# Kernel tuning notes

Measured on AMD Instinct MI355X. Metric: run time of the kernel, lower is better.

Reference implementation:

```python
import jax, jax.numpy as jnp
import numpy as np

N = 4096        # nodes
C = 256         # in_channels
E0 = 65536      # edges before adding self-loops
RATIO = 0.5
K = int(np.ceil(RATIO * N))   # pooled nodes (topk)
NEG = 0.2       # leaky relu negative slope


def setup_inputs() -> dict:
    key = jax.random.key(0)
    ks = jax.random.split(key, 12)
    x = jax.random.normal(ks[0], (N, C), jnp.float32)
    src = jax.random.randint(ks[1], (E0,), 0, N)
    off = jax.random.randint(ks[2], (E0,), 1, N)
    dst = (src + off) % N                      # guaranteed no self-loops
    edge_index = jnp.stack([src, dst]).astype(jnp.int32)
    s = 1.0 / np.sqrt(C)
    s2 = 1.0 / np.sqrt(2 * C)
    u = lambda k, shape, b: jax.random.uniform(k, shape, jnp.float32, -b, b)
    return dict(
        x=x, edge_index=edge_index,
        Wq=u(ks[3], (C, C), s), bq=u(ks[4], (C,), s),          # lin_q
        gat_w=u(ks[5], (2 * C,), s2), gat_b=u(ks[6], (1,), s2),  # gat_att
        le1_w=u(ks[7], (C,), s), le1_b=u(ks[8], (1,), s),      # LEConv lin1
        le2_w=u(ks[9], (C,), s),                                # LEConv lin2 (no bias)
        le3_w=u(ks[10], (C,), s), le3_b=u(ks[11], (1,), s),    # LEConv lin3
    )


def _asap(x, edge_index, Wq, bq, gat_w, gat_b, le1_w, le1_b, le2_w, le3_w, le3_b):
    # add_remaining_self_loops (inputs have none -> all N loops, weight 1)
    loops = jnp.arange(N, dtype=edge_index.dtype)
    ei = jnp.concatenate([edge_index, jnp.stack([loops, loops])], axis=1)
    i, j = ei[0], ei[1]          # i: aggregation target, j: neighbor

    x_pool = x                   # GNN is None -> x_pool = x
    xj = x_pool[j]               # [E, C]

    # Master2Token attention: X_q = scatter_max over target i
    Xq = jax.ops.segment_max(xj, i, num_segments=N)       # [N, C]
    Mq = Xq @ Wq + bq                                     # lin_q
    sc = jnp.concatenate([Mq[i], xj], axis=-1) @ gat_w + gat_b[0]  # [E]
    sc = jnp.where(sc > 0, sc, NEG * sc)                  # leaky relu

    # segment softmax over targets i
    m = jax.ops.segment_max(sc, i, num_segments=N)
    e = jnp.exp(sc - m[i])
    z = jax.ops.segment_sum(e, i, num_segments=N)
    score = e / z[i]                                      # dropout_att=0, eval

    # cluster representation
    out = jax.ops.segment_sum(x[j] * score[:, None], i, num_segments=N)  # [N, C]

    # fitness = sigmoid(LEConv(out)): x_i' = lin3(x_i) + sum_j (lin1(x_j) - lin2(x_i))
    a = out @ le1_w + le1_b[0]                            # [N]
    b = out @ le2_w                                       # [N]
    agg = jax.ops.segment_sum(a[j] - b[i], i, num_segments=N)
    fitness = jax.nn.sigmoid(agg + out @ le3_w + le3_b[0])  # [N]

    # topk pooling (single graph -> global top_k)
    fit_k, perm = jax.lax.top_k(fitness, K)
    x_out = out[perm] * fit_k[:, None]                    # [K, C]

    # graph_connectivity: E = S^T A S (dense stand-in for coalesce+spspmm)
    n_idx = jnp.zeros(N, jnp.int32).at[perm].set(jnp.arange(K, dtype=jnp.int32))
    in_perm = jnp.zeros(N, bool).at[perm].set(True)
    sS = jax.lax.stop_gradient(score) * in_perm[i]        # score.detach(), kept-cluster edges
    S = jnp.zeros((N, K), x.dtype).at[j, n_idx[i]].add(sS)   # S[j, new(i)] = score
    A = jnp.zeros((N, N), x.dtype).at[i, j].add(1.0)      # edge_weight None -> ones, coalesced
    Eadj = S.T @ (A @ S)                                  # [K, K]
    # remove_self_loops then add_remaining_self_loops(fill=1)
    Eadj = Eadj - jnp.diag(jnp.diag(Eadj)) + jnp.eye(K, dtype=Eadj.dtype)
    return x_out, Eadj, perm


def reference(x, edge_index, Wq, bq, gat_w, gat_b, le1_w, le1_b, le2_w, le3_w, le3_b):
    return _asap(x, edge_index, Wq, bq, gat_w, gat_b,
                 le1_w, le1_b, le2_w, le3_w, le3_b)
```

## Files before the change

### kernel.cpp

```cpp
#include <hip/hip_runtime.h>
#include <math.h>

constexpr int NN  = 4096;
constexpr int CC  = 256;
constexpr int EE0 = 65536;
constexpr int EE  = 69632;
constexpr int KK  = 2048;
constexpr int SL  = 128;

__device__ __forceinline__ void edge_ij(const int* __restrict__ ei, int e, int& i, int& j) {
    if (e < EE0) { i = ei[e]; j = ei[EE0 + e]; }
    else         { i = e - EE0; j = i; }
}

__global__ __launch_bounds__(256) void k_build(const int* __restrict__ ei,
                                               int* cnt_i, int* cnt_j,
                                               int* lsti_j, int* slot_ij, int* lstj_i,
                                               const float* __restrict__ x,
                                               const float* __restrict__ Wq, const float* __restrict__ bq,
                                               const float* __restrict__ gat_w, const float* __restrict__ gat_b,
                                               double* wv, double* consts, double* beta_node, int EB) {
    const int t = threadIdx.x, g = t >> 6, l = t & 63;
    if ((int)blockIdx.x < EB) {
        int e = blockIdx.x * 256 + t;
        if (e >= EE) return;
        int i, j; edge_ij(ei, e, i, j);
        int si = atomicAdd(&cnt_i[i], 1);
        int sj = atomicAdd(&cnt_j[j], 1);
        lsti_j[i * SL + si]  = j;
        slot_ij[i * SL + si] = j * SL + sj;
        lstj_i[j * SL + sj]  = i;
        return;
    }
    if ((int)blockIdx.x < EB + CC) {
        int k = blockIdx.x - EB;
        double s = (double)Wq[k * CC + t] * (double)gat_w[t];
        #pragma unroll
        for (int d = 32; d > 0; d >>= 1) s += __shfl_down(s, d, 64);
        __shared__ double red[4];
        if (l == 0) red[g] = s;
        __syncthreads();
        if (t == 0) wv[k] = red[0] + red[1] + red[2] + red[3];
        if (k == 0 && t == 0) {
            double cb = 0.0;
            for (int q = 0; q < CC; ++q) cb += (double)bq[q] * (double)gat_w[q];
            consts[0] = cb + (double)gat_b[0];
        }
        return;
    }
    int m = (blockIdx.x - EB - CC) * 4 + g;
    const float* gw2 = gat_w + CC;
    float4 v = ((const float4*)(x + (size_t)m * CC))[l];
    double s = (double)v.x * (double)gw2[4 * l]     + (double)v.y * (double)gw2[4 * l + 1]
             + (double)v.z * (double)gw2[4 * l + 2] + (double)v.w * (double)gw2[4 * l + 3];
    #pragma unroll
    for (int d = 32; d > 0; d >>= 1) s += __shfl_down(s, d, 64);
    if (l == 0) beta_node[m] = s;
}

__global__ __launch_bounds__(256) void k_attn(const float* __restrict__ x,
                                              const int* __restrict__ cnt_i, const int* __restrict__ lsti_j,
                                              const int* __restrict__ slot_ij,
                                              const int* __restrict__ cnt_j, const int* __restrict__ lstj_i,
                                              const double* __restrict__ wv, const double* __restrict__ beta_node,
                                              const double* __restrict__ consts,
                                              const float* __restrict__ le1_w, const float* __restrict__ le1_b,
                                              const float* __restrict__ le2_w,
                                              const float* __restrict__ le3_w, const float* __restrict__ le3_b,
                                              float* __restrict__ sval_i, float* __restrict__ svalj,
                                              float* __restrict__ out32,
                                              double* __restrict__ zlog) {
    __shared__ int    sj[SL];
    __shared__ double ssc[SL];
    __shared__ double mz[2];
    __shared__ double bcast;
    __shared__ union { float4 m4[4][64]; double d[4][CC]; } red;

    const int n = blockIdx.x, t = threadIdx.x, g = t >> 6, l = t & 63;
    const int base = n * SL;
    const int deg = cnt_i[n];

    for (int p = t; p < deg; p += 256) {
        int j = lsti_j[base + p];
        sj[p] = j;
        ssc[p] = beta_node[j];
    }
    __syncthreads();

    float4 mx = make_float4(-INFINITY, -INFINITY, -INFINITY, -INFINITY);
    for (int p = g; p < deg; p += 4) {
        float4 v = ((const float4*)(x + (size_t)sj[p] * CC))[l];
        mx.x = fmaxf(mx.x, v.x); mx.y = fmaxf(mx.y, v.y);
        mx.z = fmaxf(mx.z, v.z); mx.w = fmaxf(mx.w, v.w);
    }
    red.m4[g][l] = mx;
    __syncthreads();
    if (g == 0) {
        float4 a = red.m4[0][l], b = red.m4[1][l], c2 = red.m4[2][l], d4 = red.m4[3][l];
        float m0 = fmaxf(fmaxf(a.x, b.x), fmaxf(c2.x, d4.x));
        float m1 = fmaxf(fmaxf(a.y, b.y), fmaxf(c2.y, d4.y));
        float m2 = fmaxf(fmaxf(a.z, b.z), fmaxf(c2.z, d4.z));
        float m3 = fmaxf(fmaxf(a.w, b.w), fmaxf(c2.w, d4.w));
        double alph = (double)m0 * wv[4 * l]     + (double)m1 * wv[4 * l + 1]
                    + (double)m2 * wv[4 * l + 2] + (double)m3 * wv[4 * l + 3];
        #pragma unroll
        for (int dd = 32; dd > 0; dd >>= 1) alph += __shfl_down(alph, dd, 64);
        if (l == 0) mz[0] = alph + consts[0];
    }
    __syncthreads();
    double an = mz[0];
    for (int p = t; p < deg; p += 256) {
        double v = an + ssc[p];
        ssc[p] = v > 0.0 ? v : 0.2 * v;
    }
    __syncthreads();
    if (t < 64) {
        double mm = -1e300;
        for (int p = l; p < deg; p += 64) mm = fmax(mm, ssc[p]);
        #pragma unroll
        for (int d = 32; d > 0; d >>= 1) mm = fmax(mm, __shfl_xor(mm, d, 64));
        double z = 0.0;
        for (int p = l; p < deg; p += 64) z += exp(ssc[p] - mm);
        #pragma unroll
        for (int d = 32; d > 0; d >>= 1) z += __shfl_xor(z, d, 64);
        if (l == 0) { mz[0] = mm; mz[1] = 1.0 / z; }
    }
    __syncthreads();
    double mm = mz[0], inv = mz[1];
    for (int p = t; p < deg; p += 256) {
        double sc = exp(ssc[p] - mm) * inv;
        ssc[p] = sc;
        float scf = (float)sc;
        sval_i[base + p] = scf;
        svalj[slot_ij[base + p]] = scf;
    }
    __syncthreads();
    double a0 = 0, a1 = 0, a2 = 0, a3 = 0;
    for (int p = g; p < deg; p += 4) {
        double sc = ssc[p];
        float4 v = ((const float4*)(x + (size_t)sj[p] * CC))[l];
        a0 += sc * (double)v.x; a1 += sc * (double)v.y;
        a2 += sc * (double)v.z; a3 += sc * (double)v.w;
    }
    red.d[g][4 * l + 0] = a0; red.d[g][4 * l + 1] = a1;
    red.d[g][4 * l + 2] = a2; red.d[g][4 * l + 3] = a3;
    __syncthreads();
    if (g == 0) {
        double o0 = red.d[0][4*l]   + red.d[1][4*l]   + red.d[2][4*l]   + red.d[3][4*l];
        double o1 = red.d[0][4*l+1] + red.d[1][4*l+1] + red.d[2][4*l+1] + red.d[3][4*l+1];
        double o2 = red.d[0][4*l+2] + red.d[1][4*l+2] + red.d[2][4*l+2] + red.d[3][4*l+2];
        double o3 = red.d[0][4*l+3] + red.d[1][4*l+3] + red.d[2][4*l+3] + red.d[3][4*l+3];
        float4 ov; ov.x = (float)o0; ov.y = (float)o1; ov.z = (float)o2; ov.w = (float)o3;
        ((float4*)(out32 + (size_t)n * CC))[l] = ov;
        float4 w1 = ((const float4*)le1_w)[l];
        float4 w2 = ((const float4*)le2_w)[l];
        float4 w3 = ((const float4*)le3_w)[l];
        double s1 = o0 * (double)w1.x + o1 * (double)w1.y + o2 * (double)w1.z + o3 * (double)w1.w;
        double s2 = o0 * (double)w2.x + o1 * (double)w2.y + o2 * (double)w2.z + o3 * (double)w2.w;
        double s3 = o0 * (double)w3.x + o1 * (double)w3.y + o2 * (double)w3.z + o3 * (double)w3.w;
        #pragma unroll
        for (int dd = 32; dd > 0; dd >>= 1) {
            s1 += __shfl_down(s1, dd, 64);
            s2 += __shfl_down(s2, dd, 64);
            s3 += __shfl_down(s3, dd, 64);
        }
        if (l == 0) {
            double a64n = s1 + (double)le1_b[0];
            double b64n = s2;
            double l3vn = s3 + (double)le3_b[0];
            atomicAdd(&zlog[n], l3vn - (double)deg * b64n);
            bcast = a64n;
        }
    }
    __syncthreads();
    double a64n = bcast;
    int cj = cnt_j[n], jb = n * SL;
    for (int p = t; p < cj; p += 256) {
        atomicAdd(&zlog[lstj_i[jb + p]], a64n);
    }
}

__global__ __launch_bounds__(256) void k_rank(const double* __restrict__ zlog,
                                              const float* __restrict__ out32,
                                              int* __restrict__ perm, int* __restrict__ n_idx,
                                              float* __restrict__ xout, float* __restrict__ operm) {
    int n = blockIdx.x, t = threadIdx.x;
    double zn = zlog[n];
    int cnt = 0;
    #pragma unroll
    for (int u = 0; u < NN / 256; ++u) {
        int m = t + u * 256;
        double zm = zlog[m];
        cnt += ((zm > zn) || (zm == zn && m < n)) ? 1 : 0;
    }
    #pragma unroll
    for (int d = 32; d > 0; d >>= 1) cnt += __shfl_down(cnt, d, 64);
    __shared__ int red[4];
    __shared__ int rr;
    if ((t & 63) == 0) red[t >> 6] = cnt;
    __syncthreads();
    if (t == 0) {
        int r = red[0] + red[1] + red[2] + red[3];
        rr = r;
        if (r < KK) {
            perm[r] = n;
            n_idx[n] = r;
            operm[r] = (float)n;
        } else {
            n_idx[n] = -1;
        }
    }
    __syncthreads();
    int r = rr;
    if (r < KK) {
        double fit = 1.0 / (1.0 + exp(-zn));
        xout[(size_t)r * CC + t] = (float)((double)out32[(size_t)n * CC + t] * fit);
    }
}

__global__ __launch_bounds__(256) void k_eadj(const int* __restrict__ cnt_i, const int* __restrict__ lsti_j,
                                              const float* __restrict__ sval_i,
                                              const int* __restrict__ cnt_j, const int* __restrict__ lstj_i,
                                              const float* __restrict__ svalj,
                                              const int* __restrict__ n_idx,
                                              const int* __restrict__ perm,
                                              float* __restrict__ Ead) {
    __shared__ float row[KK];
    int r = blockIdx.x, t = threadIdx.x;
    float4 z4 = make_float4(0.f, 0.f, 0.f, 0.f);
    for (int c = t; c < KK / 4; c += 256) ((float4*)row)[c] = z4;
    __syncthreads();
    int n = perm[r];
    int deg = cnt_i[n];
    int base = n * SL;
    int grp = t >> 5, lane = t & 31;
    for (int p = grp; p < deg; p += 8) {
        int j = lsti_j[base + p];
        float s1 = sval_i[base + p];
        int cj = cnt_j[j], jb = j * SL;
        for (int q = lane; q < cj; q += 32) {
            int c = n_idx[lstj_i[jb + q]];
            if (c >= 0) atomicAdd(&row[c], s1 * svalj[jb + q]);
        }
    }
    __syncthreads();
    float* __restrict__ erow = Ead + (size_t)r * KK;
    for (int c4 = t; c4 < KK / 4; c4 += 256) {
        float4 v = ((float4*)row)[c4];
        int base4 = c4 * 4;
        int dr = r - base4;
        if (dr >= 0 && dr < 4) ((float*)&v)[dr] = 1.0f;
        ((float4*)erow)[c4] = v;
    }
}

extern "C" void kernel_launch(void* const* d_in, const int* in_sizes, int n_in,
                              void* d_out, int out_size, void* d_ws, size_t ws_size,
                              hipStream_t stream) {
    const float* x     = (const float*)d_in[0];
    const int*   ei    = (const int*)d_in[1];
    const float* Wq    = (const float*)d_in[2];
    const float* bq    = (const float*)d_in[3];
    const float* gat_w = (const float*)d_in[4];
    const float* gat_b = (const float*)d_in[5];
    const float* le1_w = (const float*)d_in[6];
    const float* le1_b = (const float*)d_in[7];
    const float* le2_w = (const float*)d_in[8];
    const float* le3_w = (const float*)d_in[9];
    const float* le3_b = (const float*)d_in[10];

    float* xout  = (float*)d_out;
    float* Ead   = xout + (size_t)KK * CC;
    float* operm = Ead + (size_t)KK * KK;

    char* w = (char*)d_ws;
    auto alloc = [&](size_t bytes) -> void* {
        void* p = (void*)w;
        w += (bytes + 255) & ~(size_t)255;
        return p;
    };
    int*    cnt_i  = (int*)alloc(NN * 4);
    int*    cnt_j  = (int*)alloc(NN * 4);
    double* zlog   = (double*)alloc(NN * 8);
    float*  out32  = (float*)alloc((size_t)NN * CC * 4);
    double* beta_node = (double*)alloc(NN * 8);
    double* wv     = (double*)alloc(CC * 8);
    double* consts = (double*)alloc(64);
    int*   lsti_j  = (int*)alloc((size_t)NN * SL * 4);
    int*   slot_ij = (int*)alloc((size_t)NN * SL * 4);
    int*   lstj_i  = (int*)alloc((size_t)NN * SL * 4);
    float* sval_i  = (float*)alloc((size_t)NN * SL * 4);
    float* svalj   = (float*)alloc((size_t)NN * SL * 4);
    int*   n_idx   = (int*)alloc(NN * 4);
    int*   perm    = (int*)alloc(KK * 4);

    hipMemsetAsync(cnt_i, 0, 2 * NN * 4 + NN * 8, stream);

    const int EB = (EE + 255) / 256;

    k_build<<<EB + CC + NN / 4, 256, 0, stream>>>(ei, cnt_i, cnt_j,
                                                  lsti_j, slot_ij, lstj_i, x,
                                                  Wq, bq, gat_w, gat_b, wv, consts, beta_node, EB);
    k_attn<<<NN, 256, 0, stream>>>(x, cnt_i, lsti_j, slot_ij, cnt_j, lstj_i,
                                   wv, beta_node, consts,
                                   le1_w, le1_b, le2_w, le3_w, le3_b,
                                   sval_i, svalj, out32, zlog);
    k_rank<<<NN, 256, 0, stream>>>(zlog, out32, perm, n_idx, xout, operm);
    k_eadj<<<KK, 256, 0, stream>>>(cnt_i, lsti_j, sval_i, cnt_j, lstj_i, svalj,
                                   n_idx, perm, Ead);
}
```

Measured before the change: 152.6 us.

## Map one wavefront per node in attention kernel, replacing shared memory with shuffles

The attention kernel now gives each node a single 64-lane wavefront instead of a 256-thread block, with four nodes per block. Neighbor indices and scores stay in registers (two per lane, for degree up to 128) and are broadcast with shuffles, which removes shared memory and block barriers. The gather loops are unrolled by four with separate accumulators to keep more loads in flight. This cuts synchronization overhead but serializes each node's neighbor loop within one wave. It assumes degree never exceeds 128, the same SL limit as before.

```diff
diff --git a/kernel.cpp b/kernel.cpp
--- a/kernel.cpp
+++ b/kernel.cpp
@@ -70,112 +70,145 @@
                                               float* __restrict__ sval_i, float* __restrict__ svalj,
                                               float* __restrict__ out32,
                                               double* __restrict__ zlog) {
-    __shared__ int    sj[SL];
-    __shared__ double ssc[SL];
-    __shared__ double mz[2];
-    __shared__ double bcast;
-    __shared__ union { float4 m4[4][64]; double d[4][CC]; } red;
-
-    const int n = blockIdx.x, t = threadIdx.x, g = t >> 6, l = t & 63;
+    const int n = (blockIdx.x << 2) + (threadIdx.x >> 6);
+    const int l = threadIdx.x & 63;
     const int base = n * SL;
     const int deg = cnt_i[n];
 
-    for (int p = t; p < deg; p += 256) {
-        int j = lsti_j[base + p];
-        sj[p] = j;
-        ssc[p] = beta_node[j];
-    }
-    __syncthreads();
+    int j0 = 0, j1 = 0;
+    double b0 = 0.0, b1 = 0.0;
+    if (l < deg)      { j0 = lsti_j[base + l];      b0 = beta_node[j0]; }
+    if (l + 64 < deg) { j1 = lsti_j[base + l + 64]; b1 = beta_node[j1]; }
 
     float4 mx = make_float4(-INFINITY, -INFINITY, -INFINITY, -INFINITY);
-    for (int p = g; p < deg; p += 4) {
-        float4 v = ((const float4*)(x + (size_t)sj[p] * CC))[l];
-        mx.x = fmaxf(mx.x, v.x); mx.y = fmaxf(mx.y, v.y);
-        mx.z = fmaxf(mx.z, v.z); mx.w = fmaxf(mx.w, v.w);
-    }
-    red.m4[g][l] = mx;
-    __syncthreads();
-    if (g == 0) {
-        float4 a = red.m4[0][l], b = red.m4[1][l], c2 = red.m4[2][l], d4 = red.m4[3][l];
-        float m0 = fmaxf(fmaxf(a.x, b.x), fmaxf(c2.x, d4.x));
-        float m1 = fmaxf(fmaxf(a.y, b.y), fmaxf(c2.y, d4.y));
-        float m2 = fmaxf(fmaxf(a.z, b.z), fmaxf(c2.z, d4.z));
-        float m3 = fmaxf(fmaxf(a.w, b.w), fmaxf(c2.w, d4.w));
-        double alph = (double)m0 * wv[4 * l]     + (double)m1 * wv[4 * l + 1]
-                    + (double)m2 * wv[4 * l + 2] + (double)m3 * wv[4 * l + 3];
-        #pragma unroll
-        for (int dd = 32; dd > 0; dd >>= 1) alph += __shfl_down(alph, dd, 64);
-        if (l == 0) mz[0] = alph + consts[0];
-    }
-    __syncthreads();
-    double an = mz[0];
-    for (int p = t; p < deg; p += 256) {
-        double v = an + ssc[p];
-        ssc[p] = v > 0.0 ? v : 0.2 * v;
-    }
-    __syncthreads();
-    if (t < 64) {
-        double mm = -1e300;
-        for (int p = l; p < deg; p += 64) mm = fmax(mm, ssc[p]);
-        #pragma unroll
-        for (int d = 32; d > 0; d >>= 1) mm = fmax(mm, __shfl_xor(mm, d, 64));
-        double z = 0.0;
-        for (int p = l; p < deg; p += 64) z += exp(ssc[p] - mm);
-        #pragma unroll
-        for (int d = 32; d > 0; d >>= 1) z += __shfl_xor(z, d, 64);
-        if (l == 0) { mz[0] = mm; mz[1] = 1.0 / z; }
-    }
-    __syncthreads();
-    double mm = mz[0], inv = mz[1];
-    for (int p = t; p < deg; p += 256) {
-        double sc = exp(ssc[p] - mm) * inv;
-        ssc[p] = sc;
-        float scf = (float)sc;
-        sval_i[base + p] = scf;
-        svalj[slot_ij[base + p]] = scf;
-    }
-    __syncthreads();
-    double a0 = 0, a1 = 0, a2 = 0, a3 = 0;
-    for (int p = g; p < deg; p += 4) {
-        double sc = ssc[p];
-        float4 v = ((const float4*)(x + (size_t)sj[p] * CC))[l];
-        a0 += sc * (double)v.x; a1 += sc * (double)v.y;
-        a2 += sc * (double)v.z; a3 += sc * (double)v.w;
-    }
-    red.d[g][4 * l + 0] = a0; red.d[g][4 * l + 1] = a1;
-    red.d[g][4 * l + 2] = a2; red.d[g][4 * l + 3] = a3;
-    __syncthreads();
-    if (g == 0) {
-        double o0 = red.d[0][4*l]   + red.d[1][4*l]   + red.d[2][4*l]   + red.d[3][4*l];
-        double o1 = red.d[0][4*l+1] + red.d[1][4*l+1] + red.d[2][4*l+1] + red.d[3][4*l+1];
-        double o2 = red.d[0][4*l+2] + red.d[1][4*l+2] + red.d[2][4*l+2] + red.d[3][4*l+2];
-        double o3 = red.d[0][4*l+3] + red.d[1][4*l+3] + red.d[2][4*l+3] + red.d[3][4*l+3];
-        float4 ov; ov.x = (float)o0; ov.y = (float)o1; ov.z = (float)o2; ov.w = (float)o3;
-        ((float4*)(out32 + (size_t)n * CC))[l] = ov;
-        float4 w1 = ((const float4*)le1_w)[l];
-        float4 w2 = ((const float4*)le2_w)[l];
-        float4 w3 = ((const float4*)le3_w)[l];
-        double s1 = o0 * (double)w1.x + o1 * (double)w1.y + o2 * (double)w1.z + o3 * (double)w1.w;
-        double s2 = o0 * (double)w2.x + o1 * (double)w2.y + o2 * (double)w2.z + o3 * (double)w2.w;
-        double s3 = o0 * (double)w3.x + o1 * (double)w3.y + o2 * (double)w3.z + o3 * (double)w3.w;
-        #pragma unroll
-        for (int dd = 32; dd > 0; dd >>= 1) {
-            s1 += __shfl_down(s1, dd, 64);
-            s2 += __shfl_down(s2, dd, 64);
-            s3 += __shfl_down(s3, dd, 64);
-        }
-        if (l == 0) {
-            double a64n = s1 + (double)le1_b[0];
-            double b64n = s2;
-            double l3vn = s3 + (double)le3_b[0];
-            atomicAdd(&zlog[n], l3vn - (double)deg * b64n);
-            bcast = a64n;
-        }
-    }
-    __syncthreads();
-    double a64n = bcast;
+    for (int p4 = 0; p4 < deg; p4 += 4) {
+        {   int p = p4;
+            int jp = __shfl(p < 64 ? j0 : j1, p & 63, 64);
+            float4 v = ((const float4*)(x + (size_t)jp * CC))[l];
+            mx.x = fmaxf(mx.x, v.x); mx.y = fmaxf(mx.y, v.y);
+            mx.z = fmaxf(mx.z, v.z); mx.w = fmaxf(mx.w, v.w);
+        }
+        if (p4 + 1 < deg) { int p = p4 + 1;
+            int jp = __shfl(p < 64 ? j0 : j1, p & 63, 64);
+            float4 v = ((const float4*)(x + (size_t)jp * CC))[l];
+            mx.x = fmaxf(mx.x, v.x); mx.y = fmaxf(mx.y, v.y);
+            mx.z = fmaxf(mx.z, v.z); mx.w = fmaxf(mx.w, v.w);
+        }
+        if (p4 + 2 < deg) { int p = p4 + 2;
+            int jp = __shfl(p < 64 ? j0 : j1, p & 63, 64);
+            float4 v = ((const float4*)(x + (size_t)jp * CC))[l];
+            mx.x = fmaxf(mx.x, v.x); mx.y = fmaxf(mx.y, v.y);
+            mx.z = fmaxf(mx.z, v.z); mx.w = fmaxf(mx.w, v.w);
+        }
+        if (p4 + 3 < deg) { int p = p4 + 3;
+            int jp = __shfl(p < 64 ? j0 : j1, p & 63, 64);
+            float4 v = ((const float4*)(x + (size_t)jp * CC))[l];
+            mx.x = fmaxf(mx.x, v.x); mx.y = fmaxf(mx.y, v.y);
+            mx.z = fmaxf(mx.z, v.z); mx.w = fmaxf(mx.w, v.w);
+        }
+    }
+
+    double al = (double)mx.x * wv[4 * l]     + (double)mx.y * wv[4 * l + 1]
+              + (double)mx.z * wv[4 * l + 2] + (double)mx.w * wv[4 * l + 3];
+    #pragma unroll
+    for (int d = 32; d > 0; d >>= 1) al += __shfl_down(al, d, 64);
+    double an = __shfl(al, 0, 64) + consts[0];
+
+    double s0 = 0.0, s1 = 0.0;
+    if (l < deg)      { double v = an + b0; s0 = v > 0.0 ? v : 0.2 * v; }
+    if (l + 64 < deg) { double v = an + b1; s1 = v > 0.0 ? v : 0.2 * v; }
+    double mm = -1e300;
+    if (l < deg)      mm = fmax(mm, s0);
+    if (l + 64 < deg) mm = fmax(mm, s1);
+    #pragma unroll
+    for (int d = 32; d > 0; d >>= 1) mm = fmax(mm, __shfl_xor(mm, d, 64));
+    double z = 0.0;
+    if (l < deg)      z += exp(s0 - mm);
+    if (l + 64 < deg) z += exp(s1 - mm);
+    #pragma unroll
+    for (int d = 32; d > 0; d >>= 1) z += __shfl_xor(z, d, 64);
+    double inv = 1.0 / z;
+
+    double sc0 = 0.0, sc1 = 0.0;
+    if (l < deg) {
+        sc0 = exp(s0 - mm) * inv;
+        float scf = (float)sc0;
+        sval_i[base + l] = scf;
+        svalj[slot_ij[base + l]] = scf;
+    }
+    if (l + 64 < deg) {
+        sc1 = exp(s1 - mm) * inv;
+        float scf = (float)sc1;
+        sval_i[base + l + 64] = scf;
+        svalj[slot_ij[base + l + 64]] = scf;
+    }
+
+    double A0x = 0, A0y = 0, A0z = 0, A0w = 0;
+    double A1x = 0, A1y = 0, A1z = 0, A1w = 0;
+    double A2x = 0, A2y = 0, A2z = 0, A2w = 0;
+    double A3x = 0, A3y = 0, A3z = 0, A3w = 0;
+    for (int p4 = 0; p4 < deg; p4 += 4) {
+        {   int p = p4;
+            double sc = __shfl(p < 64 ? sc0 : sc1, p & 63, 64);
+            int jp = __shfl(p < 64 ? j0 : j1, p & 63, 64);
+            float4 v = ((const float4*)(x + (size_t)jp * CC))[l];
+            A0x += sc * (double)v.x; A0y += sc * (double)v.y;
+            A0z += sc * (double)v.z; A0w += sc * (double)v.w;
+        }
+        if (p4 + 1 < deg) { int p = p4 + 1;
+            double sc = __shfl(p < 64 ? sc0 : sc1, p & 63, 64);
+            int jp = __shfl(p < 64 ? j0 : j1, p & 63, 64);
+            float4 v = ((const float4*)(x + (size_t)jp * CC))[l];
+            A1x += sc * (double)v.x; A1y += sc * (double)v.y;
+            A1z += sc * (double)v.z; A1w += sc * (double)v.w;
+        }
+        if (p4 + 2 < deg) { int p = p4 + 2;
+            double sc = __shfl(p < 64 ? sc0 : sc1, p & 63, 64);
+            int jp = __shfl(p < 64 ? j0 : j1, p & 63, 64);
+            float4 v = ((const float4*)(x + (size_t)jp * CC))[l];
+            A2x += sc * (double)v.x; A2y += sc * (double)v.y;
+            A2z += sc * (double)v.z; A2w += sc * (double)v.w;
+        }
+        if (p4 + 3 < deg) { int p = p4 + 3;
+            double sc = __shfl(p < 64 ? sc0 : sc1, p & 63, 64);
+            int jp = __shfl(p < 64 ? j0 : j1, p & 63, 64);
+            float4 v = ((const float4*)(x + (size_t)jp * CC))[l];
+            A3x += sc * (double)v.x; A3y += sc * (double)v.y;
+            A3z += sc * (double)v.z; A3w += sc * (double)v.w;
+        }
+    }
+    double o0 = A0x + A1x + A2x + A3x;
+    double o1 = A0y + A1y + A2y + A3y;
+    double o2 = A0z + A1z + A2z + A3z;
+    double o3 = A0w + A1w + A2w + A3w;
+
+    float4 ov; ov.x = (float)o0; ov.y = (float)o1; ov.z = (float)o2; ov.w = (float)o3;
+    ((float4*)(out32 + (size_t)n * CC))[l] = ov;
+
+    float4 w1 = ((const float4*)le1_w)[l];
+    float4 w2 = ((const float4*)le2_w)[l];
+    float4 w3 = ((const float4*)le3_w)[l];
+    double t1 = o0 * (double)w1.x + o1 * (double)w1.y + o2 * (double)w1.z + o3 * (double)w1.w;
+    double t2 = o0 * (double)w2.x + o1 * (double)w2.y + o2 * (double)w2.z + o3 * (double)w2.w;
+    double t3 = o0 * (double)w3.x + o1 * (double)w3.y + o2 * (double)w3.z + o3 * (double)w3.w;
+    #pragma unroll
+    for (int d = 32; d > 0; d >>= 1) {
+        t1 += __shfl_down(t1, d, 64);
+        t2 += __shfl_down(t2, d, 64);
+        t3 += __shfl_down(t3, d, 64);
+    }
+    double a64n;
+    if (l == 0) {
+        double a64_ = t1 + (double)le1_b[0];
+        double b64_ = t2;
+        double l3v_ = t3 + (double)le3_b[0];
+        atomicAdd(&zlog[n], l3v_ - (double)deg * b64_);
+        a64n = a64_;
+    }
+    a64n = __shfl(a64n, 0, 64);
+
     int cj = cnt_j[n], jb = n * SL;
-    for (int p = t; p < cj; p += 256) {
+    for (int p = l; p < cj; p += 64) {
         atomicAdd(&zlog[lstj_i[jb + p]], a64n);
     }
 }
@@ -301,10 +334,10 @@
     k_build<<<EB + CC + NN / 4, 256, 0, stream>>>(ei, cnt_i, cnt_j,
                                                   lsti_j, slot_ij, lstj_i, x,
                                                   Wq, bq, gat_w, gat_b, wv, consts, beta_node, EB);
-    k_attn<<<NN, 256, 0, stream>>>(x, cnt_i, lsti_j, slot_ij, cnt_j, lstj_i,
-                                   wv, beta_node, consts,
-                                   le1_w, le1_b, le2_w, le3_w, le3_b,
-                                   sval_i, svalj, out32, zlog);
+    k_attn<<<NN / 4, 256, 0, stream>>>(x, cnt_i, lsti_j, slot_ij, cnt_j, lstj_i,
+                                       wv, beta_node, consts,
+                                       le1_w, le1_b, le2_w, le3_w, le3_b,
+                                       sval_i, svalj, out32, zlog);
     k_rank<<<NN, 256, 0, stream>>>(zlog, out32, perm, n_idx, xout, operm);
     k_eadj<<<KK, 256, 0, stream>>>(cnt_i, lsti_j, sval_i, cnt_j, lstj_i, svalj,
                                    n_idx, perm, Ead);
```

Measured after the change: 144.4 us. 1.06x faster.
